# Kernel tuning notes

Hardware: AMD Instinct MI355X
Metric: run time of the kernel (lower is better)

## Reference

```python
import jax, jax.numpy as jnp
import numpy as np

B, T, C = 2, 2048, 2048
NH, NKV, HD = 16, 4, 128
GATE_CH = 12
WINDOW = 1024


def apply_rotary_emb(x, cos, sin):
    # x: (B,T,H,HD); cos/sin: (1,T,1,HD//2)
    d = x.shape[3] // 2
    x1, x2 = x[..., :d], x[..., d:]
    return jnp.concatenate([x1 * cos + x2 * sin, -x1 * sin + x2 * cos], axis=3)


def rms_norm(x):
    return x * jax.lax.rsqrt(jnp.mean(jnp.square(x), axis=-1, keepdims=True) + 1e-06)


def setup_inputs() -> dict:
    key = jax.random.key(0)
    ks = jax.random.split(key, 7)
    # realistic RoPE tables
    theta = 10000.0 ** (-jnp.arange(HD // 2, dtype=jnp.float32) / (HD // 2))
    ang = jnp.arange(T, dtype=jnp.float32)[:, None] * theta[None, :]
    cos = jnp.cos(ang)[None, :, None, :]
    sin = jnp.sin(ang)[None, :, None, :]
    return {
        "x": jax.random.normal(ks[0], (B, T, C), jnp.float32),
        "ve": jax.random.normal(ks[1], (B, T, NKV * HD), jnp.float32),
        "cos": cos,
        "sin": sin,
        "Wq": 0.02 * jax.random.normal(ks[2], (NH * HD, C), jnp.float32),
        "Wk": 0.02 * jax.random.normal(ks[3], (NKV * HD, C), jnp.float32),
        "Wv": 0.02 * jax.random.normal(ks[4], (NKV * HD, C), jnp.float32),
        "Wproj": 0.02 * jax.random.normal(ks[5], (C, C), jnp.float32),
        "Wgate": 0.02 * jax.random.normal(ks[6], (NKV, GATE_CH), jnp.float32),
        "window_size": WINDOW,
    }


def reference(x, ve, cos, sin, Wq, Wk, Wv, Wproj, Wgate, window_size):
    B_, T_, C_ = x.shape
    q = (x @ Wq.T).reshape(B_, T_, NH, HD)
    k = (x @ Wk.T).reshape(B_, T_, NKV, HD)
    v = (x @ Wv.T).reshape(B_, T_, NKV, HD)
    # value-embedding gate-add
    gate = 3.0 * jax.nn.sigmoid(x[..., :GATE_CH] @ Wgate.T)  # (B,T,NKV)
    v = v + gate[..., None] * ve.reshape(B_, T_, NKV, HD)
    # RoPE + QK RMSNorm + scale
    q = rms_norm(apply_rotary_emb(q, cos, sin)) * 1.2
    k = rms_norm(apply_rotary_emb(k, cos, sin)) * 1.2
    # GQA head-repeat
    rep = NH // NKV
    k = jnp.repeat(k, rep, axis=2)
    v = jnp.repeat(v, rep, axis=2)
    # sliding-window causal bias (window_size > 0 branch)
    r = jnp.arange(T_)
    mask = (r[None, :] <= r[:, None]) & (r[:, None] - r[None, :] <= window_size)
    bias = jnp.where(mask, 0.0, jnp.finfo(x.dtype).min)  # (T,T)
    scores = jnp.einsum("bthd,bshd->bhts", q, k) * (1.0 / np.sqrt(HD).astype(np.float32))
    scores = scores + bias[None, None, :, :]
    w = jax.nn.softmax(scores, axis=-1)
    y = jnp.einsum("bhts,bshd->bthd", w, v).reshape(B_, T_, -1)
    return y @ Wproj.T
```

## Files before the change

### kernel.cpp

```cpp
#include <hip/hip_runtime.h>
#include <hip/hip_bf16.h>

#define BB   2
#define TT   2048
#define CC   2048
#define NHq  16
#define NKVq 4
#define HDq  128
#define ROWS (BB*TT)
#define NQKV (NHq*HDq + 2*NKVq*HDq)

using bf16 = __hip_bfloat16;
using short8  = __attribute__((ext_vector_type(8))) short;
using short4v = __attribute__((ext_vector_type(4))) short;
using f32x4   = __attribute__((ext_vector_type(4))) float;

#define MFMA16(a,b,c) __builtin_amdgcn_mfma_f32_16x16x32_bf16((a),(b),(c),0,0,0)

__device__ __forceinline__ void gll16(const bf16* g, void* l) {
    __builtin_amdgcn_global_load_lds((const __attribute__((address_space(1))) void*)g,
                                     (__attribute__((address_space(3))) void*)l,
                                     16, 0, 0);
}

__global__ void cast_all(const float* __restrict__ x,  const float* __restrict__ wq,
                         const float* __restrict__ wk, const float* __restrict__ wv,
                         const float* __restrict__ wp, bf16* __restrict__ dst) {
    long e = ((long)blockIdx.x * 256 + threadIdx.x) * 4;
    const float* src; long off;
    if (e < 8388608L)       { src = x;  off = e; }
    else if (e < 12582912L) { src = wq; off = e - 8388608L; }
    else if (e < 13631488L) { src = wk; off = e - 12582912L; }
    else if (e < 14680064L) { src = wv; off = e - 13631488L; }
    else                    { src = wp; off = e - 14680064L; }
    float4 v = *reinterpret_cast<const float4*>(src + off);
    ushort4 o;
    o.x = __bfloat16_as_ushort(__float2bfloat16(v.x));
    o.y = __bfloat16_as_ushort(__float2bfloat16(v.y));
    o.z = __bfloat16_as_ushort(__float2bfloat16(v.z));
    o.w = __bfloat16_as_ushort(__float2bfloat16(v.w));
    *reinterpret_cast<ushort4*>(dst + e) = o;
}

template<int OUT_F32>
__global__ __launch_bounds__(256) void gemm_bt(const bf16* __restrict__ A,
                                               const bf16* __restrict__ B,
                                               void* __restrict__ Cp,
                                               int M, int N, int K) {
    const int bm = blockIdx.x * 128;
    const int bn = blockIdx.y * 128;
    const int tid = threadIdx.x;
    const int lane = tid & 63;
    const int w = tid >> 6;
    const int wr = w >> 1, wc = w & 1;

    __shared__ __align__(16) bf16 As[128 * 32];
    __shared__ __align__(16) bf16 Bs[128 * 32];

    f32x4 acc[4][4];
#pragma unroll
    for (int i = 0; i < 4; ++i)
#pragma unroll
        for (int j = 0; j < 4; ++j) acc[i][j] = f32x4{0.f, 0.f, 0.f, 0.f};

    const int srow = tid >> 2;
    const int scol = (tid & 3) * 8;

    for (int k0 = 0; k0 < K; k0 += 32) {
        __syncthreads();
#pragma unroll
        for (int p = 0; p < 2; ++p) {
            gll16(&A[(size_t)(bm + p * 64 + srow) * K + k0 + scol], (char*)As + p * 4096 + tid * 16);
            gll16(&B[(size_t)(bn + p * 64 + srow) * K + k0 + scol], (char*)Bs + p * 4096 + tid * 16);
        }
        __syncthreads();

        const int fr = lane & 15;
        const int kq = (lane >> 4) * 8;
        short8 af[4], bfr[4];
#pragma unroll
        for (int m = 0; m < 4; ++m)
            af[m] = *reinterpret_cast<const short8*>(&As[(wr * 64 + m * 16 + fr) * 32 + kq]);
#pragma unroll
        for (int n = 0; n < 4; ++n)
            bfr[n] = *reinterpret_cast<const short8*>(&Bs[(wc * 64 + n * 16 + fr) * 32 + kq]);
#pragma unroll
        for (int m = 0; m < 4; ++m)
#pragma unroll
            for (int n = 0; n < 4; ++n)
                acc[m][n] = MFMA16(af[m], bfr[n], acc[m][n]);
    }

    const int cr = (lane >> 4) * 4;
    const int cc = lane & 15;
#pragma unroll
    for (int m = 0; m < 4; ++m)
#pragma unroll
        for (int n = 0; n < 4; ++n) {
            int row = bm + wr * 64 + m * 16 + cr;
            int col = bn + wc * 64 + n * 16 + cc;
#pragma unroll
            for (int j = 0; j < 4; ++j) {
                float v = acc[m][n][j];
                if (OUT_F32) ((float*)Cp)[(size_t)(row + j) * N + col] = v;
                else         ((bf16*)Cp)[(size_t)(row + j) * N + col] = __float2bfloat16(v);
            }
        }
}

__global__ __launch_bounds__(256) void postproc(const float* __restrict__ x,
                                                const float* __restrict__ ve,
                                                const float* __restrict__ cosb,
                                                const float* __restrict__ sinb,
                                                const float* __restrict__ Wgate,
                                                bf16* __restrict__ qkv) {
    const int row = blockIdx.x;
    const int t = row & (TT - 1);
    const int tid = threadIdx.x;
    __shared__ float gate_s[NKVq];
    if (tid < NKVq) {
        float g = 0.f;
#pragma unroll
        for (int c = 0; c < 12; ++c) g += x[(size_t)row * CC + c] * Wgate[tid * 12 + c];
        gate_s[tid] = 3.0f / (1.0f + __expf(-g));
    }
    __syncthreads();

    bf16* qkvr = qkv + (size_t)row * NQKV;

#pragma unroll
    for (int i = 0; i < 2; ++i) {
        int idx = tid + i * 256;
        float v = __bfloat162float(qkvr[2560 + idx]);
        v += gate_s[idx >> 7] * ve[(size_t)row * 512 + idx];
        qkvr[2560 + idx] = __float2bfloat16(v);
    }

    const int lane = tid & 63;
    const int w = tid >> 6;
    const float cv = cosb[(size_t)t * 64 + lane];
    const float sv = sinb[(size_t)t * 64 + lane];
    for (int hh = w; hh < NHq + NKVq; hh += 4) {
        int off = (hh < NHq) ? hh * HDq : 2048 + (hh - NHq) * HDq;
        float x1 = __bfloat162float(qkvr[off + lane]);
        float x2 = __bfloat162float(qkvr[off + 64 + lane]);
        float r1 =  x1 * cv + x2 * sv;
        float r2 = -x1 * sv + x2 * cv;
        float ss = r1 * r1 + r2 * r2;
#pragma unroll
        for (int m = 1; m < 64; m <<= 1) ss += __shfl_xor(ss, m);
        float sc = rsqrtf(ss * (1.0f / 128.0f) + 1e-6f) * 1.2f;
        qkvr[off + lane]      = __float2bfloat16(r1 * sc);
        qkvr[off + 64 + lane] = __float2bfloat16(r2 * sc);
    }
}

__global__ __launch_bounds__(256, 2) void attn_mfma(const bf16* __restrict__ qkv,
                                                    bf16* __restrict__ y,
                                                    const int* __restrict__ winp) {
    const int bid = blockIdx.x;
    const int group = bid >> 8, idx = bid & 255;
    const int bh = idx >> 3, jj = idx & 7;
    const int qt = group ? jj : (15 - jj);
    const int h = bh & 15, b = bh >> 4;
    const int t0 = qt * 128;
    const int kvh = h >> 2;
    const int tid = threadIdx.x;
    const int lane = tid & 63;
    const int w = tid >> 6;
    const int window = winp[0];

    __shared__ __align__(16) bf16 Ks[2][64 * 128];
    __shared__ __align__(16) bf16 Vt[128 * 64];
    __shared__ __align__(16) bf16 Ps[4][32 * 64];

    const int fr = lane & 15;
    const int kq = (lane >> 4) * 8;
    const int hi = lane >> 4;

    short8 qf[2][4];
#pragma unroll
    for (int mi = 0; mi < 2; ++mi) {
        const bf16* qp = qkv + ((size_t)(b * TT) + t0 + w * 32 + mi * 16 + fr) * NQKV + h * HDq;
#pragma unroll
        for (int c = 0; c < 4; ++c)
            qf[mi][c] = *reinterpret_cast<const short8*>(&qp[c * 32 + kq]);
    }

    f32x4 acc[2][8];
#pragma unroll
    for (int mi = 0; mi < 2; ++mi)
#pragma unroll
        for (int n = 0; n < 8; ++n) acc[mi][n] = f32x4{0.f, 0.f, 0.f, 0.f};
    float m2[2][4], lrow[2][4];
#pragma unroll
    for (int mi = 0; mi < 2; ++mi)
#pragma unroll
        for (int j = 0; j < 4; ++j) { m2[mi][j] = -1e30f; lrow[mi][j] = 0.f; }

    int s_lo = t0 - window; if (s_lo < 0) s_lo = 0; s_lo &= ~63;
    const int s_end = t0 + 128;

    const bf16* Kg = qkv + (size_t)b * TT * NQKV + 2048 + kvh * HDq;
    const bf16* Vg = Kg + 512;

    const int str = tid >> 4;
    const int sti = tid & 15;
    const int vf  = tid & 15;
    const int vdc = (tid >> 4) * 8;
    const float scl2 = 0.08838834764831845f * 1.4426950408889634f;
    const float THR2 = 11.54f;

    short8 vr[4];

#pragma unroll
    for (int p = 0; p < 4; ++p) {
        int row = p * 16 + str;
        int c16 = sti ^ (row & 7);
        gll16(&Kg[(size_t)(s_lo + row) * NQKV + c16 * 8], (char*)Ks + p * 4096 + tid * 16);
    }
#pragma unroll
    for (int i = 0; i < 4; ++i)
        vr[i] = *reinterpret_cast<const short8*>(&Vg[(size_t)(s_lo + 16 * i + vf) * NQKV + vdc]);
#pragma unroll
    for (int j = 0; j < 8; ++j) {
        short4v col;
        col[0] = vr[0][j]; col[1] = vr[1][j]; col[2] = vr[2][j]; col[3] = vr[3][j];
        *reinterpret_cast<short4v*>((char*)Vt + (vdc + j) * 128 + ((8 * vf) ^ (j << 4))) = col;
    }
    __syncthreads();

    int cur = 0;
    for (int sk = s_lo; sk < s_end; sk += 64) {
        const bool hn = (sk + 64 < s_end);
        if (hn) {
#pragma unroll
            for (int p = 0; p < 4; ++p) {
                int row = p * 16 + str;
                int c16 = sti ^ (row & 7);
                gll16(&Kg[(size_t)(sk + 64 + row) * NQKV + c16 * 8],
                      (char*)Ks + (cur ^ 1) * 16384 + p * 4096 + tid * 16);
            }
#pragma unroll
            for (int i = 0; i < 4; ++i)
                vr[i] = *reinterpret_cast<const short8*>(&Vg[(size_t)(sk + 64 + 16 * i + vf) * NQKV + vdc]);
        }

        f32x4 S[2][4];
#pragma unroll
        for (int mi = 0; mi < 2; ++mi)
#pragma unroll
            for (int n = 0; n < 4; ++n) S[mi][n] = f32x4{0.f, 0.f, 0.f, 0.f};
        __builtin_amdgcn_s_setprio(1);
#pragma unroll
        for (int n = 0; n < 4; ++n) {
            int rb = n * 16 + fr;
#pragma unroll
            for (int c = 0; c < 4; ++c) {
                int colb = c * 64 + kq * 2;
                short8 kf = *reinterpret_cast<const short8*>(
                    (const char*)Ks + cur * 16384 + rb * 256 + (colb ^ ((rb & 7) << 4)));
                S[0][n] = MFMA16(qf[0][c], kf, S[0][n]);
                S[1][n] = MFMA16(qf[1][c], kf, S[1][n]);
            }
        }
        __builtin_amdgcn_s_setprio(0);

        const int rw0 = t0 + w * 32;
        const bool interior = (sk + 63 <= rw0) && (rw0 + 31 - sk <= window);
#pragma unroll
        for (int mi = 0; mi < 2; ++mi) {
#pragma unroll
            for (int j = 0; j < 4; ++j) {
                const int rl = hi * 4 + j;
                float s0, s1, s2, s3;
                if (interior) {
                    s0 = S[mi][0][j] * scl2; s1 = S[mi][1][j] * scl2;
                    s2 = S[mi][2][j] * scl2; s3 = S[mi][3][j] * scl2;
                } else {
                    const int r = rw0 + mi * 16 + rl;
                    int c0 = sk + fr, c1 = c0 + 16, c2 = c0 + 32, c3 = c0 + 48;
                    s0 = (c0 <= r && r - c0 <= window) ? S[mi][0][j] * scl2 : -1e30f;
                    s1 = (c1 <= r && r - c1 <= window) ? S[mi][1][j] * scl2 : -1e30f;
                    s2 = (c2 <= r && r - c2 <= window) ? S[mi][2][j] * scl2 : -1e30f;
                    s3 = (c3 <= r && r - c3 <= window) ? S[mi][3][j] * scl2 : -1e30f;
                }
                float pm = fmaxf(fmaxf(s0, s1), fmaxf(s2, s3));
                if (!__all(pm <= m2[mi][j] + THR2)) {
                    float pr = pm;
#pragma unroll
                    for (int mm = 1; mm < 16; mm <<= 1) pr = fmaxf(pr, __shfl_xor(pr, mm));
                    float nm = fmaxf(m2[mi][j], pr);
                    float corr = exp2f(m2[mi][j] - nm);
                    m2[mi][j] = nm;
                    lrow[mi][j] *= corr;
#pragma unroll
                    for (int n = 0; n < 8; ++n) acc[mi][n][j] *= corr;
                }
                float p0 = exp2f(s0 - m2[mi][j]);
                float p1 = exp2f(s1 - m2[mi][j]);
                float p2 = exp2f(s2 - m2[mi][j]);
                float p3 = exp2f(s3 - m2[mi][j]);
                if (!interior) {
                    p0 = (s0 > -1e29f) ? p0 : 0.f;
                    p1 = (s1 > -1e29f) ? p1 : 0.f;
                    p2 = (s2 > -1e29f) ? p2 : 0.f;
                    p3 = (s3 > -1e29f) ? p3 : 0.f;
                }
                lrow[mi][j] += (p0 + p1) + (p2 + p3);
                short4v pk;
                pk[0] = (short)__bfloat16_as_ushort(__float2bfloat16(p0));
                pk[1] = (short)__bfloat16_as_ushort(__float2bfloat16(p1));
                pk[2] = (short)__bfloat16_as_ushort(__float2bfloat16(p2));
                pk[3] = (short)__bfloat16_as_ushort(__float2bfloat16(p3));
                const int prow = mi * 16 + rl;
                *reinterpret_cast<short4v*>(
                    (char*)Ps + w * 4096 + prow * 128 + ((8 * fr) ^ ((prow & 7) << 4))) = pk;
            }
        }

        __builtin_amdgcn_s_setprio(1);
#pragma unroll
        for (int c2 = 0; c2 < 2; ++c2) {
            short8 pa0 = *reinterpret_cast<const short8*>(
                (char*)Ps + w * 4096 + fr * 128 + ((c2 * 64 + hi * 16) ^ ((fr & 7) << 4)));
            short8 pa1 = *reinterpret_cast<const short8*>(
                (char*)Ps + w * 4096 + (16 + fr) * 128 + ((c2 * 64 + hi * 16) ^ ((fr & 7) << 4)));
#pragma unroll
            for (int n = 0; n < 8; ++n) {
                short8 vb = *reinterpret_cast<const short8*>(
                    (char*)Vt + (n * 16 + fr) * 128 + ((c2 * 64 + hi * 16) ^ ((fr & 7) << 4)));
                acc[0][n] = MFMA16(pa0, vb, acc[0][n]);
                acc[1][n] = MFMA16(pa1, vb, acc[1][n]);
            }
        }
        __builtin_amdgcn_s_setprio(0);

        __syncthreads();
        if (hn) {
#pragma unroll
            for (int j = 0; j < 8; ++j) {
                short4v col;
                col[0] = vr[0][j]; col[1] = vr[1][j]; col[2] = vr[2][j]; col[3] = vr[3][j];
                *reinterpret_cast<short4v*>((char*)Vt + (vdc + j) * 128 + ((8 * vf) ^ (j << 4))) = col;
            }
        }
        __syncthreads();
        cur ^= 1;
    }

#pragma unroll
    for (int mi = 0; mi < 2; ++mi)
#pragma unroll
        for (int j = 0; j < 4; ++j) {
            float l = lrow[mi][j];
#pragma unroll
            for (int mm = 1; mm < 16; mm <<= 1) l += __shfl_xor(l, mm);
            const int r = t0 + w * 32 + mi * 16 + hi * 4 + j;
            float inv = 1.f / l;
            bf16* yr = y + ((size_t)(b * TT) + r) * CC + h * HDq;
#pragma unroll
            for (int n = 0; n < 8; ++n)
                yr[n * 16 + fr] = __float2bfloat16(acc[mi][n][j] * inv);
        }
}

extern "C" void kernel_launch(void* const* d_in, const int* in_sizes, int n_in,
                              void* d_out, int out_size, void* d_ws, size_t ws_size,
                              hipStream_t stream) {
    const float* x     = (const float*)d_in[0];
    const float* ve    = (const float*)d_in[1];
    const float* cosb  = (const float*)d_in[2];
    const float* sinb  = (const float*)d_in[3];
    const float* Wq    = (const float*)d_in[4];
    const float* Wk    = (const float*)d_in[5];
    const float* Wv    = (const float*)d_in[6];
    const float* Wproj = (const float*)d_in[7];
    const float* Wgate = (const float*)d_in[8];
    const int*   winp  = (const int*)d_in[9];

    bf16* xb     = (bf16*)d_ws;
    bf16* wqkvb  = xb + (size_t)ROWS * CC;
    bf16* wprojb = wqkvb + (size_t)NQKV * CC;
    bf16* qkvb   = wprojb + (size_t)CC * CC;
    bf16* yb     = xb;

    cast_all<<<18432, 256, 0, stream>>>(x, Wq, Wk, Wv, Wproj, xb);

    gemm_bt<0><<<dim3(ROWS / 128, NQKV / 128), 256, 0, stream>>>(xb, wqkvb, qkvb, ROWS, NQKV, CC);

    postproc<<<ROWS, 256, 0, stream>>>(x, ve, cosb, sinb, Wgate, qkvb);

    attn_mfma<<<BB * NHq * (TT / 128), 256, 0, stream>>>(qkvb, yb, winp);

    gemm_bt<1><<<dim3(ROWS / 128, CC / 128), 256, 0, stream>>>(yb, wprojb, d_out, ROWS, CC, CC);
}
```

Measured before the change: 218.5 us.

## Double GEMM K-tile to 64 with XOR-swizzled LDS layout and MFMA priority

```diff
diff --git a/kernel.cpp b/kernel.cpp
--- a/kernel.cpp
+++ b/kernel.cpp
@@ -54,8 +54,8 @@
     const int w = tid >> 6;
     const int wr = w >> 1, wc = w & 1;
 
-    __shared__ __align__(16) bf16 As[128 * 32];
-    __shared__ __align__(16) bf16 Bs[128 * 32];
+    __shared__ __align__(16) bf16 As[128 * 64];
+    __shared__ __align__(16) bf16 Bs[128 * 64];
 
     f32x4 acc[4][4];
 #pragma unroll
@@ -63,32 +63,46 @@
 #pragma unroll
         for (int j = 0; j < 4; ++j) acc[i][j] = f32x4{0.f, 0.f, 0.f, 0.f};
 
-    const int srow = tid >> 2;
-    const int scol = (tid & 3) * 8;
-
-    for (int k0 = 0; k0 < K; k0 += 32) {
+    const int srow = tid >> 3;
+    const int sch  = tid & 7;
+
+    const int fr = lane & 15;
+    const int kq = lane >> 4;
+
+    for (int k0 = 0; k0 < K; k0 += 64) {
         __syncthreads();
 #pragma unroll
-        for (int p = 0; p < 2; ++p) {
-            gll16(&A[(size_t)(bm + p * 64 + srow) * K + k0 + scol], (char*)As + p * 4096 + tid * 16);
-            gll16(&B[(size_t)(bn + p * 64 + srow) * K + k0 + scol], (char*)Bs + p * 4096 + tid * 16);
+        for (int i = 0; i < 4; ++i) {
+            int row = i * 32 + srow;
+            int c = sch ^ (row & 7);
+            gll16(&A[(size_t)(bm + row) * K + k0 + c * 8], (char*)As + i * 4096 + tid * 16);
+            gll16(&B[(size_t)(bn + row) * K + k0 + c * 8], (char*)Bs + i * 4096 + tid * 16);
         }
         __syncthreads();
 
-        const int fr = lane & 15;
-        const int kq = (lane >> 4) * 8;
-        short8 af[4], bfr[4];
-#pragma unroll
-        for (int m = 0; m < 4; ++m)
-            af[m] = *reinterpret_cast<const short8*>(&As[(wr * 64 + m * 16 + fr) * 32 + kq]);
-#pragma unroll
-        for (int n = 0; n < 4; ++n)
-            bfr[n] = *reinterpret_cast<const short8*>(&Bs[(wc * 64 + n * 16 + fr) * 32 + kq]);
-#pragma unroll
-        for (int m = 0; m < 4; ++m)
-#pragma unroll
-            for (int n = 0; n < 4; ++n)
-                acc[m][n] = MFMA16(af[m], bfr[n], acc[m][n]);
+#pragma unroll
+        for (int kk = 0; kk < 2; ++kk) {
+            short8 af[4], bfr[4];
+#pragma unroll
+            for (int m = 0; m < 4; ++m) {
+                int r = wr * 64 + m * 16 + fr;
+                af[m] = *reinterpret_cast<const short8*>(
+                    (const char*)As + r * 128 + (((kk * 4 + kq) ^ (r & 7)) * 16));
+            }
+#pragma unroll
+            for (int n = 0; n < 4; ++n) {
+                int r = wc * 64 + n * 16 + fr;
+                bfr[n] = *reinterpret_cast<const short8*>(
+                    (const char*)Bs + r * 128 + (((kk * 4 + kq) ^ (r & 7)) * 16));
+            }
+            __builtin_amdgcn_s_setprio(1);
+#pragma unroll
+            for (int m = 0; m < 4; ++m)
+#pragma unroll
+                for (int n = 0; n < 4; ++n)
+                    acc[m][n] = MFMA16(af[m], bfr[n], acc[m][n]);
+            __builtin_amdgcn_s_setprio(0);
+        }
     }
 
     const int cr = (lane >> 4) * 4;
```

New measurement: 189.4 us. -13.3%, faster.
